# Kernel optimization log

Measured on AMD Instinct MI355X. Metric: run time of the kernel, lower is better.

The kernel has to match this reference:

```python
import jax, jax.numpy as jnp
import numpy as np

N_QUBITS = 21
N_LAYERS = 3
BATCH = 4


def _ry(state, w, theta, n):
    # Apply RY(theta) on wire w. state: (B, 2**n) real float32.
    # RY = [[cos(t/2), -sin(t/2)], [sin(t/2), cos(t/2)]] (real matrix).
    B = state.shape[0]
    s = state.reshape(B, 2 ** w, 2, 2 ** (n - w - 1))
    c = jnp.cos(theta / 2).reshape(-1, 1, 1)   # (B,1,1) or (1,1,1)
    sn = jnp.sin(theta / 2).reshape(-1, 1, 1)
    a0 = s[:, :, 0, :]
    a1 = s[:, :, 1, :]
    out = jnp.stack([c * a0 - sn * a1, sn * a0 + c * a1], axis=2)
    return out.reshape(B, -1)


def _cnot(state, c, t, n):
    # CNOT(control=c, target=t): flip target axis on the control=1 subspace.
    B = state.shape[0]
    lo, hi = (c, t) if c < t else (t, c)
    s = state.reshape(B, 2 ** lo, 2, 2 ** (hi - lo - 1), 2, 2 ** (n - hi - 1))
    ca, ta = (2, 4) if c == lo else (4, 2)
    c0 = jax.lax.index_in_dim(s, 0, axis=ca, keepdims=True)
    c1 = jnp.flip(jax.lax.index_in_dim(s, 1, axis=ca, keepdims=True), axis=ta)
    return jnp.concatenate([c0, c1], axis=ca).reshape(B, -1)


def setup_inputs() -> dict:
    key = jax.random.key(0)
    k1, k2 = jax.random.split(key)
    x = jax.random.normal(k1, (BATCH, N_QUBITS), dtype=jnp.float32)
    # TorchLayer default init: uniform in [0, 2*pi)
    weights = jax.random.uniform(k2, (N_LAYERS, N_QUBITS), dtype=jnp.float32) * (2.0 * np.pi)
    return {"x": x, "weights": weights}


def reference(x, weights):
    B, n = x.shape
    L = weights.shape[0]
    # |0...0> initial state; circuit is entirely real (RY, CNOT), so float32.
    state = jnp.zeros((B, 2 ** n), dtype=x.dtype).at[:, 0].set(1.0)
    # Input encoding: RY(x_i) on each wire.
    for i in range(n):
        state = _ry(state, i, x[:, i], n)
    # Variational layers: ring CNOTs then RY(weights[j, i]).
    for j in range(L):
        for i in range(n):
            state = _cnot(state, i, (i + 1) % n, n)
        for i in range(n):
            state = _ry(state, i, weights[j, i], n)
    # <Z_i> = P(bit_i = 0) - P(bit_i = 1)
    probs = state * state
    z = []
    for i in range(n):
        p = probs.reshape(B, 2 ** i, 2, -1).sum(axis=(1, 3))  # (B, 2)
        z.append(p[:, 0] - p[:, 1])
    return jnp.stack(z, axis=1)  # (B, n_qubits)
```

## Files before the change

### kernel.cpp

```cpp
#include <hip/hip_runtime.h>
#include <hip/hip_fp16.h>


#define NQ 21
#define SHC(q) __shfl(cv, (q)), __shfl(sv, (q))

__device__ constexpr int PH2(int slot) {
  int blk = slot >> 2;
  blk ^= ((blk >> 3) & 7) ^ ((blk >> 6) & 7);
  return (blk << 2) | (slot & 3);
}

template<int Q>
__device__ __forceinline__ void ry32(float* v, float c, float s) {
#pragma unroll
  for (int k = 0; k < 16; ++k) {
    int l0 = ((k >> Q) << (Q + 1)) | (k & ((1 << Q) - 1));
    int l1 = l0 | (1 << Q);
    float a0 = v[l0], a1 = v[l1];
    v[l0] = c * a0 - s * a1;
    v[l1] = s * a0 + c * a1;
  }
}

template<int C, int T>
__device__ __forceinline__ void cnot32(float* v) {
  constexpr int lo = (C < T) ? C : T;
  constexpr int hi = (C < T) ? T : C;
#pragma unroll
  for (int k = 0; k < 8; ++k) {
    int i1 = ((k >> lo) << (lo + 1)) | (k & ((1 << lo) - 1));
    int i2 = ((i1 >> hi) << (hi + 1)) | (i1 & ((1 << hi) - 1));
    int a = i2 | (1 << C);
    int b = a | (1 << T);
    float tmp = v[a]; v[a] = v[b]; v[b] = tmp;
  }
}

__device__ __forceinline__ void ld4(const uint2* __restrict__ g, int idx, float* dst) {
  uint2 r = g[idx];
  __half2 h0 = *reinterpret_cast<__half2*>(&r.x);
  __half2 h1 = *reinterpret_cast<__half2*>(&r.y);
  float2 f0 = __half22float2(h0), f1 = __half22float2(h1);
  dst[0] = f0.x; dst[1] = f0.y; dst[2] = f1.x; dst[3] = f1.y;
}
__device__ __forceinline__ uint2 pk4(const float* src) {
  __half2 h0 = __floats2half2_rn(src[0], src[1]);
  __half2 h1 = __floats2half2_rn(src[2], src[3]);
  uint2 r;
  r.x = *reinterpret_cast<unsigned int*>(&h0);
  r.y = *reinterpret_cast<unsigned int*>(&h1);
  return r;
}

#define A1 (tid | (rr << 9))
#define GH(l4) (((l4) & 0xF) | (t << 4) | (((l4) >> 4) << 11))

template<bool INIT>
__global__ __launch_bounds__(512, 4) void k_L(const float* __restrict__ x,
                                              const float* __restrict__ w,
                                              unsigned long long stp) {
  __shared__ __align__(16) float s[16384];
  float4* s4 = reinterpret_cast<float4*>(s);
  const int tid = threadIdx.x, lane = tid & 63;
  const int b = blockIdx.x >> 7, t = blockIdx.x & 127;
  float cv = 1.f, sv = 0.f;
  if (lane < NQ) sincosf(0.5f * w[lane], &sv, &cv);
  uint2* g2 = reinterpret_cast<uint2*>(stp) + ((size_t)b << 19) + ((size_t)t << 12);
  float v[32];
  float4* v4 = reinterpret_cast<float4*>(v);

  if (INIT) {
    float cx = 1.f, sx = 0.f;
    if (lane < NQ) sincosf(0.5f * x[b * NQ + lane], &sx, &cx);
    float Qp = 1.f;
#pragma unroll
    for (int i = 0; i < 9; ++i) {
      float cq = __shfl(cx, 18 - i), sq = __shfl(sx, 18 - i);
      Qp *= ((tid >> i) & 1) ? sq : cq;
    }
    float hfac[2];
#pragma unroll
    for (int bb = 0; bb < 2; ++bb) {
      int h = (t << 1) | bb;
      int h0 = h ^ (h >> 1);
      float p = 1.f;
#pragma unroll
      for (int j = 0; j < 8; ++j) {
        float cq = __shfl(cx, 7 - j), sq = __shfl(sx, 7 - j);
        p *= ((h0 >> j) & 1) ? sq : cq;
      }
      hfac[bb] = p;
    }
    float c20 = __shfl(cx, 20), s20 = __shfl(sx, 20);
    float c19 = __shfl(cx, 19), s19 = __shfl(sx, 19);
    float c9  = __shfl(cx, 9),  s9  = __shfl(sx, 9);
    float c8  = __shfl(cx, 8),  s8  = __shfl(sx, 8);
    float w0t[4], w1t[4];
#pragma unroll
    for (int i = 0; i < 4; ++i) {
      w0t[i] = ((i & 1) ? s20 : c20) * ((i & 2) ? s19 : c19);
      w1t[i] = ((i & 1) ? s9  : c9 ) * ((i & 2) ? s8  : c8 );
    }
#pragma unroll
    for (int r = 0; r < 32; ++r)
      v[r] = hfac[(r >> 4) & 1] * w1t[(r >> 2) & 3] * w0t[r & 3] * Qp;
  } else {
#pragma unroll
    for (int rr = 0; rr < 8; ++rr) ld4(g2, A1, v + 4 * rr);
  }
  cnot32<4, 3>(v); cnot32<3, 2>(v);
  ry32<4>(v, SHC(7)); ry32<3>(v, SHC(8));
  {
    const int pb = PH2(((tid & 31) << 2) | ((tid >> 5) & 3) | (((tid >> 7) & 3) << 9));
#pragma unroll
    for (int r = 0; r < 32; ++r)
      s[pb ^ PH2(((r & 3) << 7) | ((r >> 2) << 11))] = v[r];
  }
  __syncthreads();

  {
    const int pb = PH2(((tid & 3) << 7) | (tid & 0x7C) | ((tid >> 7) << 12));
#pragma unroll
    for (int rr = 0; rr < 8; ++rr) v4[rr] = s4[(pb ^ PH2(rr << 9)) >> 2];
  }
  cnot32<4, 3>(v); cnot32<3, 2>(v); cnot32<2, 1>(v); cnot32<1, 0>(v);
  ry32<4>(v, SHC(9)); ry32<3>(v, SHC(10)); ry32<2>(v, SHC(11)); ry32<1>(v, SHC(12));
  __syncthreads();
  {
    const int pb = PH2(((tid >> 3) & 3) | (tid & 4) | ((tid & 3) << 3) |
                       (tid & 0x60) | ((tid >> 7) << 12));
#pragma unroll
    for (int r = 0; r < 32; ++r) s[pb ^ PH2(r << 7)] = v[r];
  }
  __syncthreads();

  {
    const int pb = PH2(((tid & 3) << 3) | (tid & 4) | ((tid >> 3) << 8));
#pragma unroll
    for (int rr = 0; rr < 8; ++rr) v4[rr] = s4[(pb ^ PH2(rr << 5)) >> 2];
  }
  cnot32<4, 3>(v); cnot32<3, 2>(v); cnot32<2, 1>(v); cnot32<1, 0>(v);
  ry32<4>(v, SHC(13)); ry32<3>(v, SHC(14)); ry32<2>(v, SHC(15)); ry32<1>(v, SHC(16));
  __syncthreads();
  {
    const int pb = PH2((tid & 7) | ((tid >> 3) << 8));
#pragma unroll
    for (int r = 0; r < 32; ++r) s[pb ^ PH2(r << 3)] = v[r];
  }
  __syncthreads();

  {
    const int pb = PH2(tid << 5);
#pragma unroll
    for (int rr = 0; rr < 8; ++rr) v4[rr] = s4[(pb ^ PH2(rr << 2)) >> 2];
  }
  cnot32<3, 2>(v); cnot32<2, 1>(v); cnot32<1, 0>(v);
  ry32<3>(v, SHC(17)); ry32<2>(v, SHC(18)); ry32<1>(v, SHC(19));
  {
    uint4* g4o = reinterpret_cast<uint4*>(g2);
#pragma unroll
    for (int rr = 0; rr < 8; rr += 2) {
      uint2 lo = pk4(v + 4 * rr), hi = pk4(v + 4 * rr + 4);
      uint4 o; o.x = lo.x; o.y = lo.y; o.z = hi.x; o.w = hi.y;
      g4o[((rr | (tid << 3)) >> 1)] = o;
    }
  }
}

__global__ __launch_bounds__(512, 4) void k_H(const float* __restrict__ w,
                                              unsigned long long stp) {
  __shared__ __align__(16) float s[16384];
  float4* s4 = reinterpret_cast<float4*>(s);
  const int tid = threadIdx.x, lane = tid & 63;
  const int b = blockIdx.x >> 7, t = blockIdx.x & 127;
  float cv = 1.f, sv = 0.f;
  if (lane < NQ) sincosf(0.5f * w[lane], &sv, &cv);
  uint2* gb = reinterpret_cast<uint2*>(stp) + ((size_t)b << 19);
  float v[32];
  float4* v4 = reinterpret_cast<float4*>(v);

#pragma unroll
  for (int rr = 0; rr < 8; ++rr) ld4(gb, GH(A1), v + 4 * rr);
  cnot32<0, 4>(v);
  ry32<0>(v, SHC(20)); ry32<4>(v, SHC(0)); ry32<3>(v, SHC(1)); ry32<2>(v, SHC(2));
  cnot32<4, 3>(v); cnot32<3, 2>(v);
  {
    const int pb = PH2(((tid & 31) << 2) | ((tid >> 5) & 3) | (((tid >> 7) & 3) << 9));
#pragma unroll
    for (int r = 0; r < 32; ++r)
      s[pb ^ PH2(((r & 3) << 7) | ((r >> 2) << 11))] = v[r];
  }
  __syncthreads();

  {
    const int pb = PH2(((tid & 3) << 7) | (tid & 0x7C) | ((tid >> 7) << 12));
#pragma unroll
    for (int rr = 0; rr < 8; ++rr) v4[rr] = s4[(pb ^ PH2(rr << 9)) >> 2];
  }
  ry32<3>(v, SHC(3)); ry32<2>(v, SHC(4)); ry32<1>(v, SHC(5)); ry32<0>(v, SHC(6));
  cnot32<4, 3>(v); cnot32<3, 2>(v); cnot32<2, 1>(v); cnot32<1, 0>(v);
  __syncthreads();
  {
    const int pb = PH2((tid & 127) | ((tid >> 7) << 12));
#pragma unroll
    for (int r = 0; r < 32; ++r) s[pb ^ PH2(r << 7)] = v[r];
  }
  __syncthreads();

  {
    const int pb = PH2(((tid & 7) << 2) | ((tid >> 3) << 8));
#pragma unroll
    for (int rr = 0; rr < 8; ++rr) v4[rr] = s4[(pb ^ PH2(rr << 5)) >> 2];
  }
  cnot32<4, 3>(v);
#pragma unroll
  for (int rr = 0; rr < 8; ++rr) {
    int l4 = (tid & 7) | (rr << 3) | ((tid >> 3) << 6);
    gb[GH(l4)] = pk4(v + 4 * rr);
  }
}

__global__ __launch_bounds__(512, 4) void k_Hfin(const float* __restrict__ w,
                                                 unsigned long long stp,
                                                 float* __restrict__ partial) {
  __shared__ __align__(16) float s[16384];
  float4* s4 = reinterpret_cast<float4*>(s);
  const int tid = threadIdx.x, lane = tid & 63;
  const int b = blockIdx.x >> 7, t = blockIdx.x & 127;
  float cv = 1.f, sv = 0.f;
  if (lane < NQ) sincosf(0.5f * w[lane], &sv, &cv);
  const uint2* gb = reinterpret_cast<const uint2*>(stp) + ((size_t)b << 19);
  float v[32];
  float4* v4 = reinterpret_cast<float4*>(v);

#pragma unroll
  for (int rr = 0; rr < 8; ++rr) ld4(gb, GH(A1), v + 4 * rr);
  cnot32<0, 4>(v);
  ry32<0>(v, SHC(20)); ry32<4>(v, SHC(0)); ry32<3>(v, SHC(1)); ry32<2>(v, SHC(2));
  {
    const int pb = PH2(((tid & 31) << 2) | ((tid >> 5) & 3) | (((tid >> 7) & 3) << 9));
#pragma unroll
    for (int r = 0; r < 32; ++r)
      s[pb ^ PH2(((r & 3) << 7) | ((r >> 2) << 11))] = v[r];
  }
  __syncthreads();

  {
    const int pb = PH2(((tid & 3) << 7) | (tid & 0x7C) | ((tid >> 7) << 12));
#pragma unroll
    for (int rr = 0; rr < 8; ++rr) v4[rr] = s4[(pb ^ PH2(rr << 9)) >> 2];
  }
  __syncthreads();
  ry32<3>(v, SHC(3)); ry32<2>(v, SHC(4)); ry32<1>(v, SHC(5)); ry32<0>(v, SHC(6));

  float S = 0, aq6 = 0, aq5 = 0, aq4 = 0, aq3 = 0, aq2 = 0;
#pragma unroll
  for (int r = 0; r < 32; ++r) {
    float p = v[r] * v[r];
    S += p;
    aq6 += (r & 1)  ? -p : p;
    aq5 += (r & 2)  ? -p : p;
    aq4 += (r & 4)  ? -p : p;
    aq3 += (r & 8)  ? -p : p;
    aq2 += (r & 16) ? -p : p;
  }
  float a21[21];
  a21[6] = aq6; a21[5] = aq5; a21[4] = aq4; a21[3] = aq3; a21[2] = aq2;
  a21[20] = (tid & 1)   ? -S : S;
  a21[19] = (tid & 2)   ? -S : S;
  a21[18] = (tid & 4)   ? -S : S;
  a21[17] = (tid & 8)   ? -S : S;
  a21[16] = (tid & 16)  ? -S : S;
  a21[15] = (tid & 32)  ? -S : S;
  a21[7]  = (tid & 64)  ? -S : S;
  a21[1]  = (tid & 128) ? -S : S;
  a21[0]  = (tid & 256) ? -S : S;
  a21[14] = (t & 1)  ? -S : S;
  a21[13] = (t & 2)  ? -S : S;
  a21[12] = (t & 4)  ? -S : S;
  a21[11] = (t & 8)  ? -S : S;
  a21[10] = (t & 16) ? -S : S;
  a21[9]  = (t & 32) ? -S : S;
  a21[8]  = (t & 64) ? -S : S;

  const int wv = tid >> 6;
#pragma unroll
  for (int q = 0; q < 21; ++q) {
    float val = a21[q];
    val += __shfl_down(val, 32);
    val += __shfl_down(val, 16);
    val += __shfl_down(val, 8);
    val += __shfl_down(val, 4);
    val += __shfl_down(val, 2);
    val += __shfl_down(val, 1);
    if (lane == 0) s[q * 8 + wv] = val;
  }
  __syncthreads();
  if (tid < NQ) {
    float sum = 0.f;
#pragma unroll
    for (int k = 0; k < 8; ++k) sum += s[tid * 8 + k];
    partial[blockIdx.x * NQ + tid] = sum;
  }
}

__global__ void k_red(const float* __restrict__ partial, float* __restrict__ out) {
  __shared__ float red[84][8];
  const int tid = threadIdx.x;
  const int pair = tid >> 3, k8 = tid & 7;
  if (pair < 84) {
    int b = pair / NQ, q = pair % NQ;
    float sum = 0.f;
#pragma unroll
    for (int i = 0; i < 16; ++i) sum += partial[(b * 128 + k8 * 16 + i) * NQ + q];
    red[pair][k8] = sum;
  }
  __syncthreads();
  if (tid < 84) {
    float sum = 0.f;
#pragma unroll
    for (int k = 0; k < 8; ++k) sum += red[tid][k];
    out[tid] = sum;
  }
}

extern "C" void kernel_launch(void* const* d_in, const int* in_sizes, int n_in,
                              void* d_out, int out_size, void* d_ws, size_t ws_size,
                              hipStream_t stream) {
  const float* x = (const float*)d_in[0];
  const float* w = (const float*)d_in[1];
  float* out = (float*)d_out;
  unsigned long long stp = (unsigned long long)d_ws;
  float* partial = (float*)((char*)d_ws + (((size_t)4 << 21) * 2));
  if (ws_size < ((size_t)4 << 21) * 2 + 512 * NQ * 4) return;

  dim3 grid(512), blk(512);
  k_L<true> <<<grid, blk, 0, stream>>>(x, w +  0, stp);
  k_H       <<<grid, blk, 0, stream>>>(w +  0, stp);
  k_L<false><<<grid, blk, 0, stream>>>(nullptr, w + 21, stp);
  k_H       <<<grid, blk, 0, stream>>>(w + 21, stp);
  k_L<false><<<grid, blk, 0, stream>>>(nullptr, w + 42, stp);
  k_Hfin    <<<grid, blk, 0, stream>>>(w + 42, stp, partial);
  k_red     <<<1, dim3(672), 0, stream>>>(partial, out);
}
```

Before: 110.8 us.

## Rework shared-memory qubit permutations with vectorized LDS writes and interleaved block mapping

Replaces the scalar per-element shared-memory scatter with new bit permutations (sigma2 layouts) so that LDS stores become float2/float4 vector writes and reads use simplified swizzles. The register-to-qubit assignment changes, so gate targets, RY indices, the final <Z> bit mapping and the global store packing are all rewritten to match. The block index is remapped so that consecutive blocks interleave batch elements, which may spread memory traffic differently. This risks correctness errors in the intricate index permutations and possible new bank conflicts.

New measurement: 95.21 us. 1.16x faster.

```diff
diff --git a/kernel.cpp b/kernel.cpp
--- a/kernel.cpp
+++ b/kernel.cpp
@@ -5,10 +5,8 @@
 #define NQ 21
 #define SHC(q) __shfl(cv, (q)), __shfl(sv, (q))
 
-__device__ constexpr int PH2(int slot) {
-  int blk = slot >> 2;
-  blk ^= ((blk >> 3) & 7) ^ ((blk >> 6) & 7);
-  return (blk << 2) | (slot & 3);
+__device__ __forceinline__ int PH2B(int blk) {
+  return blk ^ ((blk >> 3) & 7) ^ ((blk >> 6) & 7);
 }
 
 template<int Q>
@@ -44,17 +42,34 @@
   float2 f0 = __half22float2(h0), f1 = __half22float2(h1);
   dst[0] = f0.x; dst[1] = f0.y; dst[2] = f1.x; dst[3] = f1.y;
 }
-__device__ __forceinline__ uint2 pk4(const float* src) {
-  __half2 h0 = __floats2half2_rn(src[0], src[1]);
-  __half2 h1 = __floats2half2_rn(src[2], src[3]);
-  uint2 r;
-  r.x = *reinterpret_cast<unsigned int*>(&h0);
-  r.y = *reinterpret_cast<unsigned int*>(&h1);
-  return r;
+__device__ __forceinline__ unsigned pkh(float a, float b) {
+  __half2 h = __floats2half2_rn(a, b);
+  return *reinterpret_cast<unsigned*>(&h);
 }
 
 #define A1 (tid | (rr << 9))
 #define GH(l4) (((l4) & 0xF) | (t << 4) | (((l4) >> 4) << 11))
+
+#define WR_SIGMA2(s, v)                                                        \
+  {                                                                            \
+    const int pbs = (((tid >> 5) & 1) << 1) | ((tid & 31) << 2) |              \
+                    (((tid >> 6) & 7) << 9);                                   \
+    _Pragma("unroll") for (int i = 0; i < 16; ++i) {                           \
+      int r = (i & 3) | ((i >> 2) << 3);                                       \
+      int sl = pbs ^ (((i & 3) << 7) | ((i >> 2) << 12));                      \
+      int a = (PH2B(sl >> 2) << 2) | (sl & 3);                                 \
+      float2 o; o.x = (v)[r]; o.y = (v)[r | 4];                                \
+      *reinterpret_cast<float2*>((s) + a) = o;                                 \
+    }                                                                          \
+  }
+
+#define RD_SIGMA2(s4, v4)                                                      \
+  {                                                                            \
+    const int pbb = (tid & 31) | (((tid >> 5) & 3) << 5) |                     \
+                    (((tid >> 7) & 3) << 10);                                  \
+    _Pragma("unroll") for (int rr = 0; rr < 8; ++rr)                           \
+      (v4)[rr] = (s4)[PH2B(pbb ^ (rr << 7))];                                  \
+  }
 
 template<bool INIT>
 __global__ __launch_bounds__(512, 4) void k_L(const float* __restrict__ x,
@@ -63,7 +78,9 @@
   __shared__ __align__(16) float s[16384];
   float4* s4 = reinterpret_cast<float4*>(s);
   const int tid = threadIdx.x, lane = tid & 63;
-  const int b = blockIdx.x >> 7, t = blockIdx.x & 127;
+  const int bid = blockIdx.x;
+  const int b = (bid & 7) >> 1;
+  const int t = ((bid >> 3) << 1) | (bid & 1);
   float cv = 1.f, sv = 0.f;
   if (lane < NQ) sincosf(0.5f * w[lane], &sv, &cv);
   uint2* g2 = reinterpret_cast<uint2*>(stp) + ((size_t)b << 19) + ((size_t)t << 12);
@@ -111,59 +128,66 @@
   }
   cnot32<4, 3>(v); cnot32<3, 2>(v);
   ry32<4>(v, SHC(7)); ry32<3>(v, SHC(8));
-  {
-    const int pb = PH2(((tid & 31) << 2) | ((tid >> 5) & 3) | (((tid >> 7) & 3) << 9));
-#pragma unroll
-    for (int r = 0; r < 32; ++r)
-      s[pb ^ PH2(((r & 3) << 7) | ((r >> 2) << 11))] = v[r];
-  }
-  __syncthreads();
-
-  {
-    const int pb = PH2(((tid & 3) << 7) | (tid & 0x7C) | ((tid >> 7) << 12));
-#pragma unroll
-    for (int rr = 0; rr < 8; ++rr) v4[rr] = s4[(pb ^ PH2(rr << 9)) >> 2];
-  }
-  cnot32<4, 3>(v); cnot32<3, 2>(v); cnot32<2, 1>(v); cnot32<1, 0>(v);
-  ry32<4>(v, SHC(9)); ry32<3>(v, SHC(10)); ry32<2>(v, SHC(11)); ry32<1>(v, SHC(12));
-  __syncthreads();
-  {
-    const int pb = PH2(((tid >> 3) & 3) | (tid & 4) | ((tid & 3) << 3) |
-                       (tid & 0x60) | ((tid >> 7) << 12));
-#pragma unroll
-    for (int r = 0; r < 32; ++r) s[pb ^ PH2(r << 7)] = v[r];
-  }
-  __syncthreads();
-
-  {
-    const int pb = PH2(((tid & 3) << 3) | (tid & 4) | ((tid >> 3) << 8));
-#pragma unroll
-    for (int rr = 0; rr < 8; ++rr) v4[rr] = s4[(pb ^ PH2(rr << 5)) >> 2];
-  }
-  cnot32<4, 3>(v); cnot32<3, 2>(v); cnot32<2, 1>(v); cnot32<1, 0>(v);
-  ry32<4>(v, SHC(13)); ry32<3>(v, SHC(14)); ry32<2>(v, SHC(15)); ry32<1>(v, SHC(16));
-  __syncthreads();
-  {
-    const int pb = PH2((tid & 7) | ((tid >> 3) << 8));
-#pragma unroll
-    for (int r = 0; r < 32; ++r) s[pb ^ PH2(r << 3)] = v[r];
-  }
-  __syncthreads();
-
-  {
-    const int pb = PH2(tid << 5);
-#pragma unroll
-    for (int rr = 0; rr < 8; ++rr) v4[rr] = s4[(pb ^ PH2(rr << 2)) >> 2];
-  }
-  cnot32<3, 2>(v); cnot32<2, 1>(v); cnot32<1, 0>(v);
-  ry32<3>(v, SHC(17)); ry32<2>(v, SHC(18)); ry32<1>(v, SHC(19));
+  WR_SIGMA2(s, v);
+  __syncthreads();
+
+  RD_SIGMA2(s4, v4);
+  cnot32<0, 4>(v); cnot32<4, 3>(v); cnot32<3, 2>(v); cnot32<2, 1>(v);
+  ry32<0>(v, SHC(9)); ry32<4>(v, SHC(10)); ry32<3>(v, SHC(11)); ry32<2>(v, SHC(12));
+  __syncthreads();
+  {
+    const int pbs = (tid & 0x1E) | ((tid & 1) << 5) | (tid & 0x40) |
+                    (((tid >> 5) & 1) << 7) | ((tid >> 7) << 12);
+#pragma unroll
+    for (int i = 0; i < 16; ++i) {
+      int r = (i & 1) | ((i >> 1) << 2);
+      int sl = pbs ^ ((((i >> 1) & 7) << 8) | ((i & 1) << 11));
+      int a = (PH2B(sl >> 2) << 2) | (sl & 3);
+      float2 o; o.x = v[r]; o.y = v[r | 2];
+      *reinterpret_cast<float2*>(s + a) = o;
+    }
+  }
+  __syncthreads();
+
+  {
+    const int pbb = ((tid & 7) << 3) | (((tid >> 3) & 7) << 6) | (((tid >> 6) & 7) << 9);
+#pragma unroll
+    for (int rr = 0; rr < 8; ++rr) v4[rr] = s4[PH2B(pbb | rr)];
+  }
+  cnot32<0, 4>(v); cnot32<4, 3>(v); cnot32<3, 2>(v); cnot32<2, 1>(v);
+  ry32<0>(v, SHC(13)); ry32<4>(v, SHC(14)); ry32<3>(v, SHC(15)); ry32<2>(v, SHC(16));
+  __syncthreads();
+  {
+    const int pbs = (((tid >> 2) & 1) << 2) | (((tid >> 1) & 1) << 3) |
+                    ((tid & 1) << 4) | (((tid >> 3) & 7) << 8) |
+                    (((tid >> 6) & 7) << 11);
+#pragma unroll
+    for (int i = 0; i < 8; ++i) {
+      int r = (i & 1) | ((i >> 1) << 3);
+      int sl = pbs ^ ((((i >> 1) & 1) << 5) | (((i >> 2) & 1) << 6) | ((i & 1) << 7));
+      int a = PH2B(sl >> 2) << 2;
+      float4 o; o.x = v[r]; o.y = v[r | 2]; o.z = v[r | 4]; o.w = v[r | 6];
+      *reinterpret_cast<float4*>(s + a) = o;
+    }
+  }
+  __syncthreads();
+
+  {
+    const int pbb = tid << 3;
+#pragma unroll
+    for (int rr = 0; rr < 8; ++rr) v4[rr] = s4[PH2B(pbb | rr)];
+  }
+  cnot32<0, 4>(v); cnot32<4, 3>(v); cnot32<3, 2>(v);
+  ry32<0>(v, SHC(17)); ry32<4>(v, SHC(18)); ry32<3>(v, SHC(19));
   {
     uint4* g4o = reinterpret_cast<uint4*>(g2);
 #pragma unroll
-    for (int rr = 0; rr < 8; rr += 2) {
-      uint2 lo = pk4(v + 4 * rr), hi = pk4(v + 4 * rr + 4);
-      uint4 o; o.x = lo.x; o.y = lo.y; o.z = hi.x; o.w = hi.y;
-      g4o[((rr | (tid << 3)) >> 1)] = o;
+    for (int i = 0; i < 4; ++i) {
+      int c = (i & 1) | ((i >> 1) << 1);
+      uint4 o;
+      o.x = pkh(v[c], v[c + 4]);   o.y = pkh(v[c + 8], v[c + 12]);
+      o.z = pkh(v[c + 16], v[c + 20]); o.w = pkh(v[c + 24], v[c + 28]);
+      g4o[(i & 1) | ((i >> 1) << 1) | (tid << 2)] = o;
     }
   }
 }
@@ -173,7 +197,9 @@
   __shared__ __align__(16) float s[16384];
   float4* s4 = reinterpret_cast<float4*>(s);
   const int tid = threadIdx.x, lane = tid & 63;
-  const int b = blockIdx.x >> 7, t = blockIdx.x & 127;
+  const int bid = blockIdx.x;
+  const int b = (bid & 7) >> 1;
+  const int t = ((bid >> 3) << 1) | (bid & 1);
   float cv = 1.f, sv = 0.f;
   if (lane < NQ) sincosf(0.5f * w[lane], &sv, &cv);
   uint2* gb = reinterpret_cast<uint2*>(stp) + ((size_t)b << 19);
@@ -185,39 +211,43 @@
   cnot32<0, 4>(v);
   ry32<0>(v, SHC(20)); ry32<4>(v, SHC(0)); ry32<3>(v, SHC(1)); ry32<2>(v, SHC(2));
   cnot32<4, 3>(v); cnot32<3, 2>(v);
-  {
-    const int pb = PH2(((tid & 31) << 2) | ((tid >> 5) & 3) | (((tid >> 7) & 3) << 9));
-#pragma unroll
-    for (int r = 0; r < 32; ++r)
-      s[pb ^ PH2(((r & 3) << 7) | ((r >> 2) << 11))] = v[r];
-  }
-  __syncthreads();
-
-  {
-    const int pb = PH2(((tid & 3) << 7) | (tid & 0x7C) | ((tid >> 7) << 12));
-#pragma unroll
-    for (int rr = 0; rr < 8; ++rr) v4[rr] = s4[(pb ^ PH2(rr << 9)) >> 2];
-  }
-  ry32<3>(v, SHC(3)); ry32<2>(v, SHC(4)); ry32<1>(v, SHC(5)); ry32<0>(v, SHC(6));
-  cnot32<4, 3>(v); cnot32<3, 2>(v); cnot32<2, 1>(v); cnot32<1, 0>(v);
-  __syncthreads();
-  {
-    const int pb = PH2((tid & 127) | ((tid >> 7) << 12));
-#pragma unroll
-    for (int r = 0; r < 32; ++r) s[pb ^ PH2(r << 7)] = v[r];
-  }
-  __syncthreads();
-
-  {
-    const int pb = PH2(((tid & 7) << 2) | ((tid >> 3) << 8));
-#pragma unroll
-    for (int rr = 0; rr < 8; ++rr) v4[rr] = s4[(pb ^ PH2(rr << 5)) >> 2];
-  }
-  cnot32<4, 3>(v);
-#pragma unroll
-  for (int rr = 0; rr < 8; ++rr) {
-    int l4 = (tid & 7) | (rr << 3) | ((tid >> 3) << 6);
-    gb[GH(l4)] = pk4(v + 4 * rr);
+  WR_SIGMA2(s, v);
+  __syncthreads();
+
+  RD_SIGMA2(s4, v4);
+  ry32<4>(v, SHC(3)); ry32<3>(v, SHC(4)); ry32<2>(v, SHC(5)); ry32<1>(v, SHC(6));
+  cnot32<0, 4>(v); cnot32<4, 3>(v); cnot32<3, 2>(v); cnot32<2, 1>(v);
+  __syncthreads();
+  {
+    const int pbs = (((tid >> 3) & 1) << 1) | (((tid >> 5) & 1) << 2) |
+                    (((tid >> 6) & 1) << 3) | (tid & 16) | ((tid & 1) << 5) |
+                    (((tid >> 1) & 1) << 6) | (((tid >> 2) & 1) << 7) |
+                    ((tid >> 7) << 12);
+#pragma unroll
+    for (int i = 0; i < 16; ++i) {
+      int r = (i & 1) | ((i >> 1) << 2);
+      int sl = pbs ^ ((((i >> 1) & 7) << 8) | ((i & 1) << 11));
+      int a = (PH2B(sl >> 2) << 2) | (sl & 3);
+      float2 o; o.x = v[r]; o.y = v[r | 2];
+      *reinterpret_cast<float2*>(s + a) = o;
+    }
+  }
+  __syncthreads();
+
+  {
+    const int pbb = ((tid & 7) << 3) | (((tid >> 3) & 7) << 6) | (((tid >> 6) & 7) << 9);
+#pragma unroll
+    for (int rr = 0; rr < 8; ++rr) v4[rr] = s4[PH2B(pbb | rr)];
+  }
+  cnot32<0, 4>(v);
+#pragma unroll
+  for (int i = 0; i < 8; ++i) {
+    int r0 = i & 1, r1 = (i >> 1) & 1, rh = (i >> 2) & 1;
+    int c = r0 | (r1 << 1) | (rh << 4);
+    int gidx = (tid & 7) | (r1 << 3) | (t << 4) |
+               ((rh | (r0 << 1) | (((tid >> 3) & 0x3F) << 2)) << 11);
+    uint2 o; o.x = pkh(v[c], v[c + 4]); o.y = pkh(v[c + 8], v[c + 12]);
+    gb[gidx] = o;
   }
 }
 
@@ -227,7 +257,9 @@
   __shared__ __align__(16) float s[16384];
   float4* s4 = reinterpret_cast<float4*>(s);
   const int tid = threadIdx.x, lane = tid & 63;
-  const int b = blockIdx.x >> 7, t = blockIdx.x & 127;
+  const int bid = blockIdx.x;
+  const int b = (bid & 7) >> 1;
+  const int t = ((bid >> 3) << 1) | (bid & 1);
   float cv = 1.f, sv = 0.f;
   if (lane < NQ) sincosf(0.5f * w[lane], &sv, &cv);
   const uint2* gb = reinterpret_cast<const uint2*>(stp) + ((size_t)b << 19);
@@ -238,42 +270,33 @@
   for (int rr = 0; rr < 8; ++rr) ld4(gb, GH(A1), v + 4 * rr);
   cnot32<0, 4>(v);
   ry32<0>(v, SHC(20)); ry32<4>(v, SHC(0)); ry32<3>(v, SHC(1)); ry32<2>(v, SHC(2));
-  {
-    const int pb = PH2(((tid & 31) << 2) | ((tid >> 5) & 3) | (((tid >> 7) & 3) << 9));
-#pragma unroll
-    for (int r = 0; r < 32; ++r)
-      s[pb ^ PH2(((r & 3) << 7) | ((r >> 2) << 11))] = v[r];
-  }
-  __syncthreads();
-
-  {
-    const int pb = PH2(((tid & 3) << 7) | (tid & 0x7C) | ((tid >> 7) << 12));
-#pragma unroll
-    for (int rr = 0; rr < 8; ++rr) v4[rr] = s4[(pb ^ PH2(rr << 9)) >> 2];
-  }
-  __syncthreads();
-  ry32<3>(v, SHC(3)); ry32<2>(v, SHC(4)); ry32<1>(v, SHC(5)); ry32<0>(v, SHC(6));
-
-  float S = 0, aq6 = 0, aq5 = 0, aq4 = 0, aq3 = 0, aq2 = 0;
+  WR_SIGMA2(s, v);
+  __syncthreads();
+
+  RD_SIGMA2(s4, v4);
+  __syncthreads();
+  ry32<4>(v, SHC(3)); ry32<3>(v, SHC(4)); ry32<2>(v, SHC(5)); ry32<1>(v, SHC(6));
+
+  float S = 0, aq2 = 0, aq6 = 0, aq5 = 0, aq4 = 0, aq3 = 0;
 #pragma unroll
   for (int r = 0; r < 32; ++r) {
     float p = v[r] * v[r];
     S += p;
-    aq6 += (r & 1)  ? -p : p;
-    aq5 += (r & 2)  ? -p : p;
-    aq4 += (r & 4)  ? -p : p;
-    aq3 += (r & 8)  ? -p : p;
-    aq2 += (r & 16) ? -p : p;
+    aq2 += (r & 1)  ? -p : p;
+    aq6 += (r & 2)  ? -p : p;
+    aq5 += (r & 4)  ? -p : p;
+    aq4 += (r & 8)  ? -p : p;
+    aq3 += (r & 16) ? -p : p;
   }
   float a21[21];
-  a21[6] = aq6; a21[5] = aq5; a21[4] = aq4; a21[3] = aq3; a21[2] = aq2;
-  a21[20] = (tid & 1)   ? -S : S;
-  a21[19] = (tid & 2)   ? -S : S;
-  a21[18] = (tid & 4)   ? -S : S;
-  a21[17] = (tid & 8)   ? -S : S;
-  a21[16] = (tid & 16)  ? -S : S;
-  a21[15] = (tid & 32)  ? -S : S;
-  a21[7]  = (tid & 64)  ? -S : S;
+  a21[2] = aq2; a21[6] = aq6; a21[5] = aq5; a21[4] = aq4; a21[3] = aq3;
+  a21[18] = (tid & 1)   ? -S : S;
+  a21[17] = (tid & 2)   ? -S : S;
+  a21[16] = (tid & 4)   ? -S : S;
+  a21[15] = (tid & 8)   ? -S : S;
+  a21[7]  = (tid & 16)  ? -S : S;
+  a21[20] = (tid & 32)  ? -S : S;
+  a21[19] = (tid & 64)  ? -S : S;
   a21[1]  = (tid & 128) ? -S : S;
   a21[0]  = (tid & 256) ? -S : S;
   a21[14] = (t & 1)  ? -S : S;
@@ -301,7 +324,7 @@
     float sum = 0.f;
 #pragma unroll
     for (int k = 0; k < 8; ++k) sum += s[tid * 8 + k];
-    partial[blockIdx.x * NQ + tid] = sum;
+    partial[((b << 7) | t) * NQ + tid] = sum;
   }
 }
 
```

## Halve per-block tile to 16 amplitudes per thread, doubling grid and occupancy

Applied to the files above, without the earlier changes.

Each block now handles 8192 amplitudes instead of 16384, with 16 registers per thread, half the shared memory, and launch bounds raised to 8 blocks per CU over a 1024-block grid. Qubit-to-pass assignment, the shared-memory swizzle (now PH3 with float2 stores) and the block-to-batch interleaving are reworked to match. The aim is higher occupancy and better latency hiding. The cost is more shared-memory transpose passes per kernel, and the partial-sum reduction must read strided block indices.

After: 131.2 us. 18.3% more time.

```diff
diff --git a/kernel.cpp b/kernel.cpp
--- a/kernel.cpp
+++ b/kernel.cpp
@@ -5,16 +5,14 @@
 #define NQ 21
 #define SHC(q) __shfl(cv, (q)), __shfl(sv, (q))
 
-__device__ constexpr int PH2(int slot) {
-  int blk = slot >> 2;
-  blk ^= ((blk >> 3) & 7) ^ ((blk >> 6) & 7);
-  return (blk << 2) | (slot & 3);
+__device__ __forceinline__ int PH3(int g) {
+  return g ^ ((g >> 3) & 7) ^ ((g >> 6) & 7) ^ ((g >> 9) & 7);
 }
 
 template<int Q>
-__device__ __forceinline__ void ry32(float* v, float c, float s) {
-#pragma unroll
-  for (int k = 0; k < 16; ++k) {
+__device__ __forceinline__ void ry16(float* v, float c, float s) {
+#pragma unroll
+  for (int k = 0; k < 8; ++k) {
     int l0 = ((k >> Q) << (Q + 1)) | (k & ((1 << Q) - 1));
     int l1 = l0 | (1 << Q);
     float a0 = v[l0], a1 = v[l1];
@@ -24,11 +22,11 @@
 }
 
 template<int C, int T>
-__device__ __forceinline__ void cnot32(float* v) {
+__device__ __forceinline__ void cnot16(float* v) {
   constexpr int lo = (C < T) ? C : T;
   constexpr int hi = (C < T) ? T : C;
 #pragma unroll
-  for (int k = 0; k < 8; ++k) {
+  for (int k = 0; k < 4; ++k) {
     int i1 = ((k >> lo) << (lo + 1)) | (k & ((1 << lo) - 1));
     int i2 = ((i1 >> hi) << (hi + 1)) | (i1 & ((1 << hi) - 1));
     int a = i2 | (1 << C);
@@ -44,30 +42,31 @@
   float2 f0 = __half22float2(h0), f1 = __half22float2(h1);
   dst[0] = f0.x; dst[1] = f0.y; dst[2] = f1.x; dst[3] = f1.y;
 }
-__device__ __forceinline__ uint2 pk4(const float* src) {
-  __half2 h0 = __floats2half2_rn(src[0], src[1]);
-  __half2 h1 = __floats2half2_rn(src[2], src[3]);
-  uint2 r;
-  r.x = *reinterpret_cast<unsigned int*>(&h0);
-  r.y = *reinterpret_cast<unsigned int*>(&h1);
-  return r;
-}
-
-#define A1 (tid | (rr << 9))
-#define GH(l4) (((l4) & 0xF) | (t << 4) | (((l4) >> 4) << 11))
+__device__ __forceinline__ unsigned pkh(float a, float b) {
+  __half2 h = __floats2half2_rn(a, b);
+  return *reinterpret_cast<unsigned*>(&h);
+}
+__device__ __forceinline__ void st2(float* s, int sl, float a, float b) {
+  int ps = (PH3(sl >> 2) << 2) | (sl & 3);
+  *reinterpret_cast<float2*>(s + ps) = float2{a, b};
+}
+
+#define GH(lg) (((lg) & 3) | (t << 2) | (((lg) >> 2) << 10))
 
 template<bool INIT>
-__global__ __launch_bounds__(512, 4) void k_L(const float* __restrict__ x,
+__global__ __launch_bounds__(512, 8) void k_L(const float* __restrict__ x,
                                               const float* __restrict__ w,
                                               unsigned long long stp) {
-  __shared__ __align__(16) float s[16384];
+  __shared__ __align__(16) float s[8192];
   float4* s4 = reinterpret_cast<float4*>(s);
   const int tid = threadIdx.x, lane = tid & 63;
-  const int b = blockIdx.x >> 7, t = blockIdx.x & 127;
+  const int bid = blockIdx.x;
+  const int b = (bid & 7) >> 1;
+  const int t = ((bid >> 3) << 1) | (bid & 1);
   float cv = 1.f, sv = 0.f;
   if (lane < NQ) sincosf(0.5f * w[lane], &sv, &cv);
-  uint2* g2 = reinterpret_cast<uint2*>(stp) + ((size_t)b << 19) + ((size_t)t << 12);
-  float v[32];
+  uint2* g2 = reinterpret_cast<uint2*>(stp) + ((size_t)b << 19) + ((size_t)t << 11);
+  float v[16];
   float4* v4 = reinterpret_cast<float4*>(v);
 
   if (INIT) {
@@ -86,8 +85,8 @@
       int h0 = h ^ (h >> 1);
       float p = 1.f;
 #pragma unroll
-      for (int j = 0; j < 8; ++j) {
-        float cq = __shfl(cx, 7 - j), sq = __shfl(sx, 7 - j);
+      for (int j = 0; j < 9; ++j) {
+        float cq = __shfl(cx, 8 - j), sq = __shfl(sx, 8 - j);
         p *= ((h0 >> j) & 1) ? sq : cq;
       }
       hfac[bb] = p;
@@ -95,194 +94,278 @@
     float c20 = __shfl(cx, 20), s20 = __shfl(sx, 20);
     float c19 = __shfl(cx, 19), s19 = __shfl(sx, 19);
     float c9  = __shfl(cx, 9),  s9  = __shfl(sx, 9);
-    float c8  = __shfl(cx, 8),  s8  = __shfl(sx, 8);
-    float w0t[4], w1t[4];
-#pragma unroll
-    for (int i = 0; i < 4; ++i) {
+    float w0t[4];
+#pragma unroll
+    for (int i = 0; i < 4; ++i)
       w0t[i] = ((i & 1) ? s20 : c20) * ((i & 2) ? s19 : c19);
-      w1t[i] = ((i & 1) ? s9  : c9 ) * ((i & 2) ? s8  : c8 );
-    }
-#pragma unroll
-    for (int r = 0; r < 32; ++r)
-      v[r] = hfac[(r >> 4) & 1] * w1t[(r >> 2) & 3] * w0t[r & 3] * Qp;
+#pragma unroll
+    for (int r = 0; r < 16; ++r)
+      v[r] = w0t[r & 3] * ((r & 4) ? s9 : c9) * hfac[(r >> 3) & 1] * Qp;
   } else {
 #pragma unroll
-    for (int rr = 0; rr < 8; ++rr) ld4(g2, A1, v + 4 * rr);
-  }
-  cnot32<4, 3>(v); cnot32<3, 2>(v);
-  ry32<4>(v, SHC(7)); ry32<3>(v, SHC(8));
-  {
-    const int pb = PH2(((tid & 31) << 2) | ((tid >> 5) & 3) | (((tid >> 7) & 3) << 9));
-#pragma unroll
-    for (int r = 0; r < 32; ++r)
-      s[pb ^ PH2(((r & 3) << 7) | ((r >> 2) << 11))] = v[r];
-  }
-  __syncthreads();
-
-  {
-    const int pb = PH2(((tid & 3) << 7) | (tid & 0x7C) | ((tid >> 7) << 12));
-#pragma unroll
-    for (int rr = 0; rr < 8; ++rr) v4[rr] = s4[(pb ^ PH2(rr << 9)) >> 2];
-  }
-  cnot32<4, 3>(v); cnot32<3, 2>(v); cnot32<2, 1>(v); cnot32<1, 0>(v);
-  ry32<4>(v, SHC(9)); ry32<3>(v, SHC(10)); ry32<2>(v, SHC(11)); ry32<1>(v, SHC(12));
-  __syncthreads();
-  {
-    const int pb = PH2(((tid >> 3) & 3) | (tid & 4) | ((tid & 3) << 3) |
-                       (tid & 0x60) | ((tid >> 7) << 12));
-#pragma unroll
-    for (int r = 0; r < 32; ++r) s[pb ^ PH2(r << 7)] = v[r];
-  }
-  __syncthreads();
-
-  {
-    const int pb = PH2(((tid & 3) << 3) | (tid & 4) | ((tid >> 3) << 8));
-#pragma unroll
-    for (int rr = 0; rr < 8; ++rr) v4[rr] = s4[(pb ^ PH2(rr << 5)) >> 2];
-  }
-  cnot32<4, 3>(v); cnot32<3, 2>(v); cnot32<2, 1>(v); cnot32<1, 0>(v);
-  ry32<4>(v, SHC(13)); ry32<3>(v, SHC(14)); ry32<2>(v, SHC(15)); ry32<1>(v, SHC(16));
-  __syncthreads();
-  {
-    const int pb = PH2((tid & 7) | ((tid >> 3) << 8));
-#pragma unroll
-    for (int r = 0; r < 32; ++r) s[pb ^ PH2(r << 3)] = v[r];
-  }
-  __syncthreads();
-
-  {
-    const int pb = PH2(tid << 5);
-#pragma unroll
-    for (int rr = 0; rr < 8; ++rr) v4[rr] = s4[(pb ^ PH2(rr << 2)) >> 2];
-  }
-  cnot32<3, 2>(v); cnot32<2, 1>(v); cnot32<1, 0>(v);
-  ry32<3>(v, SHC(17)); ry32<2>(v, SHC(18)); ry32<1>(v, SHC(19));
+    for (int rr = 0; rr < 4; ++rr) ld4(g2, tid | (rr << 9), v + 4 * rr);
+  }
+  cnot16<3, 2>(v);
+  {
+    const int bw = (((tid >> 6) & 7) << 1) | ((tid & 63) << 6);
+#pragma unroll
+    for (int i = 0; i < 8; ++i) {
+      int r = (i & 3) | ((i >> 2) << 3);
+      int sl = bw ^ ((i & 1) << 4) ^ (((i >> 1) & 1) << 5) ^ (((i >> 2) & 1) << 12);
+      st2(s, sl, v[r], v[r | 4]);
+    }
+  }
+  __syncthreads();
+
+  {
+    const int base = ((tid & 255) << 2) | ((tid >> 8) << 10);
+#pragma unroll
+    for (int rr = 0; rr < 4; ++rr) v4[rr] = s4[PH3(base ^ rr)];
+  }
+  cnot16<0, 3>(v); cnot16<3, 2>(v); cnot16<2, 1>(v);
+  ry16<0>(v, SHC(9)); ry16<3>(v, SHC(10)); ry16<2>(v, SHC(11));
+  __syncthreads();
+  {
+    const int bw = (((tid >> 5) & 7) << 1) | ((tid & 31) << 4) | ((tid >> 8) << 12);
+#pragma unroll
+    for (int i = 0; i < 8; ++i) {
+      int r = ((i & 1) << 2) | ((i & 2) << 2) | ((i >> 2) & 1);
+      int sl = bw ^ ((i & 1) << 9) ^ (((i >> 1) & 1) << 10) ^ (((i >> 2) & 1) << 11);
+      st2(s, sl, v[r], v[r | 2]);
+    }
+  }
+  __syncthreads();
+
+#pragma unroll
+  for (int rr = 0; rr < 4; ++rr) v4[rr] = s4[PH3((tid << 2) ^ rr)];
+  cnot16<0, 3>(v); cnot16<3, 2>(v); cnot16<2, 1>(v);
+  ry16<0>(v, SHC(12)); ry16<3>(v, SHC(13)); ry16<2>(v, SHC(14));
+  __syncthreads();
+  {
+    const int bw = (((tid >> 2) & 7) << 1) | ((tid & 3) << 4) | (((tid >> 5) & 15) << 9);
+#pragma unroll
+    for (int i = 0; i < 8; ++i) {
+      int r = ((i & 1) << 2) | ((i & 2) << 2) | ((i >> 2) & 1);
+      int sl = bw ^ ((i & 1) << 6) ^ (((i >> 1) & 1) << 7) ^ (((i >> 2) & 1) << 8);
+      st2(s, sl, v[r], v[r | 2]);
+    }
+  }
+  __syncthreads();
+
+#pragma unroll
+  for (int rr = 0; rr < 4; ++rr) v4[rr] = s4[PH3((tid << 2) ^ rr)];
+  cnot16<0, 3>(v); cnot16<3, 2>(v); cnot16<2, 1>(v);
+  ry16<0>(v, SHC(15)); ry16<3>(v, SHC(16)); ry16<2>(v, SHC(17));
+  __syncthreads();
+  {
+    const int bw = (((tid >> 4) & 1) << 1) | ((tid & 3) << 2) |
+                   (((tid >> 2) & 3) << 7) | (((tid >> 5) & 15) << 9);
+#pragma unroll
+    for (int i = 0; i < 8; ++i) {
+      int r = ((i & 1) << 2) | ((i & 2) << 2) | ((i >> 2) & 1);
+      int sl = bw ^ ((i & 1) << 4) ^ (((i >> 1) & 1) << 5) ^ (((i >> 2) & 1) << 6);
+      st2(s, sl, v[r], v[r | 2]);
+    }
+  }
+  __syncthreads();
+
+#pragma unroll
+  for (int rr = 0; rr < 4; ++rr) v4[rr] = s4[PH3((tid << 2) ^ rr)];
+  cnot16<0, 3>(v); cnot16<3, 2>(v);
+  ry16<0>(v, SHC(18)); ry16<3>(v, SHC(19));
   {
     uint4* g4o = reinterpret_cast<uint4*>(g2);
 #pragma unroll
-    for (int rr = 0; rr < 8; rr += 2) {
-      uint2 lo = pk4(v + 4 * rr), hi = pk4(v + 4 * rr + 4);
-      uint4 o; o.x = lo.x; o.y = lo.y; o.z = hi.x; o.w = hi.y;
-      g4o[((rr | (tid << 3)) >> 1)] = o;
-    }
-  }
-}
-
-__global__ __launch_bounds__(512, 4) void k_H(const float* __restrict__ w,
+    for (int j = 0; j < 2; ++j) {
+      int b1 = j << 1;
+      uint4 o;
+      o.x = pkh(v[b1],     v[b1 | 4]);
+      o.y = pkh(v[b1 | 8], v[b1 | 12]);
+      o.z = pkh(v[b1 | 1], v[b1 | 5]);
+      o.w = pkh(v[b1 | 9], v[b1 | 13]);
+      g4o[(tid & 31) | (j << 5) | (((tid >> 5) & 15) << 6)] = o;
+    }
+  }
+}
+
+__global__ __launch_bounds__(512, 8) void k_H(const float* __restrict__ w,
                                               unsigned long long stp) {
-  __shared__ __align__(16) float s[16384];
+  __shared__ __align__(16) float s[8192];
   float4* s4 = reinterpret_cast<float4*>(s);
   const int tid = threadIdx.x, lane = tid & 63;
-  const int b = blockIdx.x >> 7, t = blockIdx.x & 127;
+  const int bid = blockIdx.x;
+  const int b = (bid & 7) >> 1;
+  const int t = ((bid >> 3) << 1) | (bid & 1);
   float cv = 1.f, sv = 0.f;
   if (lane < NQ) sincosf(0.5f * w[lane], &sv, &cv);
   uint2* gb = reinterpret_cast<uint2*>(stp) + ((size_t)b << 19);
-  float v[32];
+  float v[16];
   float4* v4 = reinterpret_cast<float4*>(v);
 
 #pragma unroll
-  for (int rr = 0; rr < 8; ++rr) ld4(gb, GH(A1), v + 4 * rr);
-  cnot32<0, 4>(v);
-  ry32<0>(v, SHC(20)); ry32<4>(v, SHC(0)); ry32<3>(v, SHC(1)); ry32<2>(v, SHC(2));
-  cnot32<4, 3>(v); cnot32<3, 2>(v);
-  {
-    const int pb = PH2(((tid & 31) << 2) | ((tid >> 5) & 3) | (((tid >> 7) & 3) << 9));
-#pragma unroll
-    for (int r = 0; r < 32; ++r)
-      s[pb ^ PH2(((r & 3) << 7) | ((r >> 2) << 11))] = v[r];
-  }
-  __syncthreads();
-
-  {
-    const int pb = PH2(((tid & 3) << 7) | (tid & 0x7C) | ((tid >> 7) << 12));
-#pragma unroll
-    for (int rr = 0; rr < 8; ++rr) v4[rr] = s4[(pb ^ PH2(rr << 9)) >> 2];
-  }
-  ry32<3>(v, SHC(3)); ry32<2>(v, SHC(4)); ry32<1>(v, SHC(5)); ry32<0>(v, SHC(6));
-  cnot32<4, 3>(v); cnot32<3, 2>(v); cnot32<2, 1>(v); cnot32<1, 0>(v);
-  __syncthreads();
-  {
-    const int pb = PH2((tid & 127) | ((tid >> 7) << 12));
-#pragma unroll
-    for (int r = 0; r < 32; ++r) s[pb ^ PH2(r << 7)] = v[r];
-  }
-  __syncthreads();
-
-  {
-    const int pb = PH2(((tid & 7) << 2) | ((tid >> 3) << 8));
-#pragma unroll
-    for (int rr = 0; rr < 8; ++rr) v4[rr] = s4[(pb ^ PH2(rr << 5)) >> 2];
-  }
-  cnot32<4, 3>(v);
-#pragma unroll
-  for (int rr = 0; rr < 8; ++rr) {
-    int l4 = (tid & 7) | (rr << 3) | ((tid >> 3) << 6);
-    gb[GH(l4)] = pk4(v + 4 * rr);
-  }
-}
-
-__global__ __launch_bounds__(512, 4) void k_Hfin(const float* __restrict__ w,
+  for (int rr = 0; rr < 4; ++rr) ld4(gb, GH(tid | (rr << 9)), v + 4 * rr);
+  cnot16<0, 3>(v);
+  ry16<0>(v, SHC(20)); ry16<3>(v, SHC(0)); ry16<2>(v, SHC(1));
+  cnot16<3, 2>(v);
+  {
+    const int bw = (((tid >> 6) & 7) << 1) | ((tid & 63) << 6);
+#pragma unroll
+    for (int i = 0; i < 8; ++i) {
+      int r = (i & 3) | ((i >> 2) << 3);
+      int sl = bw ^ ((i & 1) << 4) ^ (((i >> 1) & 1) << 5) ^ (((i >> 2) & 1) << 12);
+      st2(s, sl, v[r], v[r | 4]);
+    }
+  }
+  __syncthreads();
+
+  {
+    const int base = ((tid & 255) << 2) | ((tid >> 8) << 10);
+#pragma unroll
+    for (int rr = 0; rr < 4; ++rr) v4[rr] = s4[PH3(base ^ rr)];
+  }
+  ry16<3>(v, SHC(2)); ry16<2>(v, SHC(3)); ry16<1>(v, SHC(4));
+  cnot16<0, 3>(v); cnot16<3, 2>(v); cnot16<2, 1>(v);
+  __syncthreads();
+  {
+    const int bw = (((tid >> 5) & 7) << 1) | ((tid & 31) << 4) | ((tid >> 8) << 12);
+#pragma unroll
+    for (int i = 0; i < 8; ++i) {
+      int r = ((i & 1) << 2) | ((i & 2) << 2) | ((i >> 2) & 1);
+      int sl = bw ^ ((i & 1) << 9) ^ (((i >> 1) & 1) << 10) ^ (((i >> 2) & 1) << 11);
+      st2(s, sl, v[r], v[r | 2]);
+    }
+  }
+  __syncthreads();
+
+#pragma unroll
+  for (int rr = 0; rr < 4; ++rr) v4[rr] = s4[PH3((tid << 2) ^ rr)];
+  ry16<3>(v, SHC(5)); ry16<2>(v, SHC(6)); ry16<1>(v, SHC(7));
+  cnot16<0, 3>(v); cnot16<3, 2>(v); cnot16<2, 1>(v);
+  __syncthreads();
+  {
+    const int bw = (((tid >> 4) & 1) << 1) | ((tid & 15) << 2) | (((tid >> 5) & 15) << 9);
+#pragma unroll
+    for (int i = 0; i < 8; ++i) {
+      int r = ((i & 1) << 2) | ((i & 2) << 2) | ((i >> 2) & 1);
+      int sl = bw ^ ((i & 1) << 6) ^ (((i >> 1) & 1) << 7) ^ (((i >> 2) & 1) << 8);
+      st2(s, sl, v[r], v[r | 2]);
+    }
+  }
+  __syncthreads();
+
+#pragma unroll
+  for (int rr = 0; rr < 4; ++rr) v4[rr] = s4[PH3((tid << 2) ^ rr)];
+  ry16<1>(v, SHC(8));
+  cnot16<0, 1>(v);
+#pragma unroll
+  for (int i = 0; i < 4; ++i) {
+    int r0b = i & 1, r1b = (i >> 1) & 1;
+    int rb = r0b | (r1b << 1);
+    int lg = (tid & 3) | (r1b << 2) | (r0b << 3) | ((tid >> 2) << 4);
+    uint2 o;
+    o.x = pkh(v[rb], v[rb | 4]);
+    o.y = pkh(v[rb | 8], v[rb | 12]);
+    gb[GH(lg)] = o;
+  }
+}
+
+__global__ __launch_bounds__(512, 8) void k_Hfin(const float* __restrict__ w,
                                                  unsigned long long stp,
                                                  float* __restrict__ partial) {
-  __shared__ __align__(16) float s[16384];
+  __shared__ __align__(16) float s[8192];
   float4* s4 = reinterpret_cast<float4*>(s);
   const int tid = threadIdx.x, lane = tid & 63;
-  const int b = blockIdx.x >> 7, t = blockIdx.x & 127;
+  const int bid = blockIdx.x;
+  const int b = (bid & 7) >> 1;
+  const int t = ((bid >> 3) << 1) | (bid & 1);
   float cv = 1.f, sv = 0.f;
   if (lane < NQ) sincosf(0.5f * w[lane], &sv, &cv);
   const uint2* gb = reinterpret_cast<const uint2*>(stp) + ((size_t)b << 19);
-  float v[32];
+  float v[16];
   float4* v4 = reinterpret_cast<float4*>(v);
 
 #pragma unroll
-  for (int rr = 0; rr < 8; ++rr) ld4(gb, GH(A1), v + 4 * rr);
-  cnot32<0, 4>(v);
-  ry32<0>(v, SHC(20)); ry32<4>(v, SHC(0)); ry32<3>(v, SHC(1)); ry32<2>(v, SHC(2));
-  {
-    const int pb = PH2(((tid & 31) << 2) | ((tid >> 5) & 3) | (((tid >> 7) & 3) << 9));
-#pragma unroll
-    for (int r = 0; r < 32; ++r)
-      s[pb ^ PH2(((r & 3) << 7) | ((r >> 2) << 11))] = v[r];
-  }
-  __syncthreads();
-
-  {
-    const int pb = PH2(((tid & 3) << 7) | (tid & 0x7C) | ((tid >> 7) << 12));
-#pragma unroll
-    for (int rr = 0; rr < 8; ++rr) v4[rr] = s4[(pb ^ PH2(rr << 9)) >> 2];
-  }
-  __syncthreads();
-  ry32<3>(v, SHC(3)); ry32<2>(v, SHC(4)); ry32<1>(v, SHC(5)); ry32<0>(v, SHC(6));
-
-  float S = 0, aq6 = 0, aq5 = 0, aq4 = 0, aq3 = 0, aq2 = 0;
-#pragma unroll
-  for (int r = 0; r < 32; ++r) {
+  for (int rr = 0; rr < 4; ++rr) ld4(gb, GH(tid | (rr << 9)), v + 4 * rr);
+  cnot16<0, 3>(v);
+  ry16<0>(v, SHC(20)); ry16<3>(v, SHC(0)); ry16<2>(v, SHC(1));
+  {
+    const int bw = (((tid >> 6) & 7) << 1) | ((tid & 63) << 6);
+#pragma unroll
+    for (int i = 0; i < 8; ++i) {
+      int r = (i & 3) | ((i >> 2) << 3);
+      int sl = bw ^ ((i & 1) << 4) ^ (((i >> 1) & 1) << 5) ^ (((i >> 2) & 1) << 12);
+      st2(s, sl, v[r], v[r | 4]);
+    }
+  }
+  __syncthreads();
+
+  {
+    const int base = ((tid & 255) << 2) | ((tid >> 8) << 10);
+#pragma unroll
+    for (int rr = 0; rr < 4; ++rr) v4[rr] = s4[PH3(base ^ rr)];
+  }
+  ry16<3>(v, SHC(2)); ry16<2>(v, SHC(3)); ry16<1>(v, SHC(4));
+  __syncthreads();
+  {
+    const int bw = (((tid >> 5) & 7) << 1) | ((tid & 31) << 4) | ((tid >> 8) << 12);
+#pragma unroll
+    for (int i = 0; i < 8; ++i) {
+      int r = ((i & 1) << 2) | ((i & 2) << 2) | ((i >> 2) & 1);
+      int sl = bw ^ ((i & 1) << 9) ^ (((i >> 1) & 1) << 10) ^ (((i >> 2) & 1) << 11);
+      st2(s, sl, v[r], v[r | 2]);
+    }
+  }
+  __syncthreads();
+
+#pragma unroll
+  for (int rr = 0; rr < 4; ++rr) v4[rr] = s4[PH3((tid << 2) ^ rr)];
+  ry16<3>(v, SHC(5)); ry16<2>(v, SHC(6)); ry16<1>(v, SHC(7));
+  __syncthreads();
+  {
+    const int bw = (((tid >> 4) & 1) << 1) | ((tid & 15) << 2) | (((tid >> 5) & 15) << 9);
+#pragma unroll
+    for (int i = 0; i < 8; ++i) {
+      int r = ((i & 1) << 2) | ((i & 2) << 2) | ((i >> 2) & 1);
+      int sl = bw ^ ((i & 1) << 6) ^ (((i >> 1) & 1) << 7) ^ (((i >> 2) & 1) << 8);
+      st2(s, sl, v[r], v[r | 2]);
+    }
+  }
+  __syncthreads();
+
+#pragma unroll
+  for (int rr = 0; rr < 4; ++rr) v4[rr] = s4[PH3((tid << 2) ^ rr)];
+  __syncthreads();
+  ry16<1>(v, SHC(8));
+
+  float S = 0, aq7 = 0, aq8 = 0, aq20 = 0, aq19 = 0;
+#pragma unroll
+  for (int r = 0; r < 16; ++r) {
     float p = v[r] * v[r];
     S += p;
-    aq6 += (r & 1)  ? -p : p;
-    aq5 += (r & 2)  ? -p : p;
-    aq4 += (r & 4)  ? -p : p;
-    aq3 += (r & 8)  ? -p : p;
-    aq2 += (r & 16) ? -p : p;
+    aq7  += (r & 1) ? -p : p;
+    aq8  += (r & 2) ? -p : p;
+    aq20 += (r & 4) ? -p : p;
+    aq19 += (r & 8) ? -p : p;
   }
   float a21[21];
-  a21[6] = aq6; a21[5] = aq5; a21[4] = aq4; a21[3] = aq3; a21[2] = aq2;
-  a21[20] = (tid & 1)   ? -S : S;
-  a21[19] = (tid & 2)   ? -S : S;
-  a21[18] = (tid & 4)   ? -S : S;
-  a21[17] = (tid & 8)   ? -S : S;
-  a21[16] = (tid & 16)  ? -S : S;
-  a21[15] = (tid & 32)  ? -S : S;
-  a21[7]  = (tid & 64)  ? -S : S;
+  a21[7] = aq7; a21[8] = aq8; a21[20] = aq20; a21[19] = aq19;
+  a21[18] = (tid & 1)   ? -S : S;
+  a21[17] = (tid & 2)   ? -S : S;
+  a21[6]  = (tid & 4)   ? -S : S;
+  a21[5]  = (tid & 8)   ? -S : S;
+  a21[4]  = (tid & 16)  ? -S : S;
+  a21[3]  = (tid & 32)  ? -S : S;
+  a21[2]  = (tid & 64)  ? -S : S;
   a21[1]  = (tid & 128) ? -S : S;
   a21[0]  = (tid & 256) ? -S : S;
-  a21[14] = (t & 1)  ? -S : S;
-  a21[13] = (t & 2)  ? -S : S;
-  a21[12] = (t & 4)  ? -S : S;
-  a21[11] = (t & 8)  ? -S : S;
-  a21[10] = (t & 16) ? -S : S;
-  a21[9]  = (t & 32) ? -S : S;
-  a21[8]  = (t & 64) ? -S : S;
+  a21[16] = (t & 1)   ? -S : S;
+  a21[15] = (t & 2)   ? -S : S;
+  a21[14] = (t & 4)   ? -S : S;
+  a21[13] = (t & 8)   ? -S : S;
+  a21[12] = (t & 16)  ? -S : S;
+  a21[11] = (t & 32)  ? -S : S;
+  a21[10] = (t & 64)  ? -S : S;
+  a21[9]  = (t & 128) ? -S : S;
 
   const int wv = tid >> 6;
 #pragma unroll
@@ -301,7 +384,7 @@
     float sum = 0.f;
 #pragma unroll
     for (int k = 0; k < 8; ++k) sum += s[tid * 8 + k];
-    partial[blockIdx.x * NQ + tid] = sum;
+    partial[bid * NQ + tid] = sum;
   }
 }
 
@@ -313,7 +396,11 @@
     int b = pair / NQ, q = pair % NQ;
     float sum = 0.f;
 #pragma unroll
-    for (int i = 0; i < 16; ++i) sum += partial[(b * 128 + k8 * 16 + i) * NQ + q];
+    for (int i = 0; i < 16; ++i) {
+      int m = k8 * 16 + i;
+      sum += partial[(((m << 3) | (2 * b + 0)) * NQ) + q];
+      sum += partial[(((m << 3) | (2 * b + 1)) * NQ) + q];
+    }
     red[pair][k8] = sum;
   }
   __syncthreads();
@@ -332,10 +419,11 @@
   const float* w = (const float*)d_in[1];
   float* out = (float*)d_out;
   unsigned long long stp = (unsigned long long)d_ws;
-  float* partial = (float*)((char*)d_ws + (((size_t)4 << 21) * 2));
-  if (ws_size < ((size_t)4 << 21) * 2 + 512 * NQ * 4) return;
-
-  dim3 grid(512), blk(512);
+  const size_t st_bytes = ((size_t)4 << 21) * 2;
+  float* partial = (float*)((char*)d_ws + st_bytes);
+  if (ws_size < st_bytes + (size_t)1024 * NQ * 4) return;
+
+  dim3 grid(1024), blk(512);
   k_L<true> <<<grid, blk, 0, stream>>>(x, w +  0, stp);
   k_H       <<<grid, blk, 0, stream>>>(w +  0, stp);
   k_L<false><<<grid, blk, 0, stream>>>(nullptr, w + 21, stp);
```
